# Kernel tuning notes

Hardware: AMD Instinct MI355X
Metric: run time of the kernel (lower is better)

Reference implementation:

```python
import jax, jax.numpy as jnp
import numpy as np

N, E, F = 50000, 400000, 32

_WN = ["w10","w11","w20","w21","w30","w31","w40","w41","wl01","wl02","wl1","wl2"]
_BN = ["b10","b11","b20","b21","b30","b31","b40","b41","bl01","bl02","bl1","bl2"]
_DIMS = [(4,F),(F,F),(2*F+F+4,F),(F,F),(6*F,F),(F,F),(6*F,F),(F,F),(F,F),(F,F),(F,4),(F,1)]


def _lin(key, fin, fout):
    kw, kb = jax.random.split(key)
    w = jax.random.normal(kw, (fin, fout), jnp.float32) / np.float32(np.sqrt(fin))
    b = jax.random.normal(kb, (fout,), jnp.float32) * 0.01
    return w, b


def setup_inputs() -> dict:
    key = jax.random.key(0)
    ks = jax.random.split(key, 5)
    inp = {}
    inp["x"] = jax.random.normal(ks[0], (N, 4), jnp.float32)
    inp["edge_index"] = jax.random.randint(ks[1], (2, E), 0, N, jnp.int32)
    inp["edge_attr"] = jax.random.normal(ks[2], (E, 4), jnp.float32)
    inp["beta"] = jax.random.normal(ks[3], (N, 3), jnp.float32)
    lkeys = jax.random.split(ks[4], len(_DIMS))
    for i, (fin, fout) in enumerate(_DIMS):
        w, b = _lin(lkeys[i], fin, fout)
        inp[_WN[i]] = w
        inp[_BN[i]] = b
    return inp


def reference(x, edge_index, edge_attr, beta,
              w10, b10, w11, b11, w20, b20, w21, b21,
              w30, b30, w31, b31, w40, b40, w41, b41,
              wl01, bl01, wl02, bl02, wl1, bl1, wl2, bl2):
    row, col = edge_index[0], edge_index[1]
    n = x.shape[0]

    def mlp2(m, w0, b0, w1, b1):
        return jax.nn.relu(m @ w0 + b0) @ w1 + b1

    def seg_mean(h):  # scatter-mean onto target nodes (row), dim_size=n
        s = jax.ops.segment_sum(h, row, num_segments=n)
        c = jax.ops.segment_sum(jnp.ones((h.shape[0], 1), h.dtype), row, num_segments=n)
        return s / jnp.maximum(c, 1.0)

    # conv1: x is zeros with dim 4 (<=5), so message = mlp0(edge_attr)
    e1 = mlp2(edge_attr, w10, b10, w11, b11)            # [E,32]
    x1 = jax.nn.relu(seg_mean(e1)); e1 = jax.nn.relu(e1)
    # conv2
    ea2 = jnp.concatenate([edge_attr, e1], axis=1)      # [E,36]
    e2 = mlp2(jnp.concatenate([x1[row], x1[col], ea2], axis=1), w20, b20, w21, b21)
    x2 = jax.nn.relu(seg_mean(e2)); e2 = jax.nn.relu(e2)
    # conv3
    x21 = jnp.concatenate([x2, x1], axis=1)             # [N,64]
    ea3 = jnp.concatenate([e2, e1], axis=1)             # [E,64]
    e3 = mlp2(jnp.concatenate([x21[row], x21[col], ea3], axis=1), w30, b30, w31, b31)
    x3 = jax.nn.relu(seg_mean(e3)); e3 = jax.nn.relu(e3)
    # conv4 (node aggregate x4 is never used downstream, so skipped)
    x32 = jnp.concatenate([x3, x2], axis=1)
    ea4 = jnp.concatenate([e3, e2], axis=1)
    e4 = jax.nn.relu(mlp2(jnp.concatenate([x32[row], x32[col], ea4], axis=1), w40, b40, w41, b41))
    # heads
    out01 = e4 @ wl01 + bl01
    out02 = e4 @ wl02 + bl02
    edge_x = out01 @ wl1 + bl1 + edge_attr
    edge_x = edge_x / jnp.maximum(jnp.linalg.norm(edge_x, axis=1, keepdims=True), 1e-12)
    probs = jax.nn.sigmoid(out02 @ wl2 + bl2)           # [E,1]
    return (probs, edge_x, beta)
```

## Files before the change

### kernel.cpp

```cpp
#include <hip/hip_runtime.h>
#include <hip/hip_bf16.h>

#define EE 400000
#define NN 50000
#define SCAN_NBLK ((NN + 1023) / 1024)
#define NTILES (EE / 16)
#define TPX (NTILES / 8)
#define NPTILES ((NN + 15) / 16)
#define INIT_NBLK ((NN + 255) / 256)

typedef float f32x4 __attribute__((ext_vector_type(4)));
typedef __bf16 bf16x8 __attribute__((ext_vector_type(8)));
typedef unsigned int u32;
typedef unsigned int u32x4 __attribute__((ext_vector_type(4)));

static __device__ __forceinline__ bf16x8 u4_as_bf8(u32x4 u) {
  return __builtin_bit_cast(bf16x8, u);
}
static __device__ __forceinline__ u32 relu_pk2(u32 d) {
  u32 m = (d & 0x80008000u) >> 15;
  m ^= 0x00010001u;
  return d & ((m << 16) - m);
}
static __device__ __forceinline__ u32 pk2bf(float a, float b) {
  union { __bf16 h[2]; u32 w; } t;
  t.h[0] = (__bf16)a; t.h[1] = (__bf16)b;
  return t.w;
}

__global__ void init_pack_kernel(const float* __restrict__ w10, const float* __restrict__ w11,
                                 const float* __restrict__ w20, const float* __restrict__ w21,
                                 const float* __restrict__ w30, const float* __restrict__ w31,
                                 const float* __restrict__ w40, const float* __restrict__ w41,
                                 const float* __restrict__ wl01, const float* __restrict__ wl1,
                                 const float* __restrict__ wl02, const float* __restrict__ wl2,
                                 const float* __restrict__ bl01, const float* __restrict__ bl02,
                                 const float* __restrict__ bl1, const float* __restrict__ bl2,
                                 __bf16* __restrict__ pk,
                                 int* __restrict__ count, float* __restrict__ headw) {
  const int t = threadIdx.x;
  if (blockIdx.x >= 43) {
    int i = (blockIdx.x - 43) * 256 + t;
    if (i < NN) count[i] = 0;
    if (blockIdx.x == 43) {
      if (t < 4) {
        float s = bl1[t];
        for (int j = 0; j < 32; ++j) s += bl01[j] * wl1[j * 4 + t];
        headw[160 + t] = s;
      } else if (t == 4) {
        float s = bl2[0];
        for (int j = 0; j < 32; ++j) s += bl02[j] * wl2[j];
        headw[164] = s;
      }
    }
    return;
  }
  const int f = blockIdx.x;
  int stage, lf;
  const float *W0, *W1;
  if (f < 4)       { stage = 1; lf = f;      W0 = w10; W1 = w11; }
  else if (f < 14) { stage = 2; lf = f - 4;  W0 = w20; W1 = w21; }
  else if (f < 28) { stage = 3; lf = f - 14; W0 = w30; W1 = w31; }
  else             { stage = 4; lf = f - 28; W0 = w40; W1 = w41; }
#pragma unroll
  for (int u = 0; u < 2; ++u) {
    int idx = t * 2 + u;
    int lane = idx >> 3, i = idx & 7;
    int l15 = lane & 15, g = lane >> 4;
    int k = 8 * g + i;
    float v = 0.f;
    if (stage == 1) {
      if (lf < 2)      v = (k < 4) ? W0[k * 32 + lf * 16 + l15] : 0.f;
      else             v = W1[k * 32 + (lf - 2) * 16 + l15];
    } else if (stage == 2) {
      if (lf < 4)      { int part = lf >> 1, nb = lf & 1; v = W0[(part * 32 + k) * 32 + nb * 16 + l15]; }
      else if (lf < 6) { int nb = lf - 4; v = (k < 4) ? W0[(64 + k) * 32 + nb * 16 + l15] : 0.f; }
      else if (lf < 8) { int nb = lf - 6; v = W0[(68 + k) * 32 + nb * 16 + l15]; }
      else             { int nb = lf - 8; v = W1[k * 32 + nb * 16 + l15]; }
    } else {
      if (lf < 8)       { int part = lf >> 2, kb = (lf >> 1) & 1, nb = lf & 1;
                          v = W0[(part * 64 + kb * 32 + k) * 32 + nb * 16 + l15]; }
      else if (lf < 12) { int eb = (lf - 8) >> 1, nb = lf & 1;
                          v = W0[(128 + eb * 32 + k) * 32 + nb * 16 + l15]; }
      else if (lf < 14) { int nb = lf - 12; v = W1[k * 32 + nb * 16 + l15]; }
      else {
        if (l15 < 4)      { float s = 0.f; for (int j = 0; j < 32; ++j) s += wl01[k * 32 + j] * wl1[j * 4 + l15]; v = s; }
        else if (l15 == 4){ float s = 0.f; for (int j = 0; j < 32; ++j) s += wl02[k * 32 + j] * wl2[j]; v = s; }
      }
    }
    pk[f * 512 + idx] = (__bf16)v;
  }
}

__global__ void hist_kernel(const int* __restrict__ rowi, int* __restrict__ count) {
  int e = blockIdx.x * blockDim.x + threadIdx.x;
  if (e < EE) atomicAdd(&count[rowi[e]], 1);
}

__global__ void scanA_kernel(const int* __restrict__ count, int* __restrict__ offs,
                             int* __restrict__ partial) {
  __shared__ int lds[1024];
  const int t = threadIdx.x;
  const int i = blockIdx.x * 1024 + t;
  int v = (i < NN) ? count[i] : 0;
  lds[t] = v;
  __syncthreads();
  for (int off = 1; off < 1024; off <<= 1) {
    int u = (t >= off) ? lds[t - off] : 0;
    __syncthreads();
    lds[t] += u;
    __syncthreads();
  }
  int incl = lds[t];
  if (i < NN) offs[i] = incl - v;
  if (t == 1023) partial[blockIdx.x] = incl;
}

__global__ void scanB_kernel(const int* __restrict__ partial, int* __restrict__ offs,
                             int* __restrict__ cursor) {
  __shared__ int sbase;
  const int t = threadIdx.x;
  const int b = blockIdx.x;
  if (t < 64) {
    int s = 0;
    for (int j = t; j < b; j += 64) s += partial[j];
#pragma unroll
    for (int o = 32; o > 0; o >>= 1) s += __shfl_down(s, o);
    if (t == 0) sbase = s;
  }
  __syncthreads();
  const int base = sbase;
  const int i = b * 1024 + t;
  if (i < NN) {
    int o = offs[i] + base;
    offs[i] = o;
    cursor[i] = o;
  }
  if (b == 0 && t == 0) offs[NN] = EE;
}

__global__ void scatter_kernel(const int* __restrict__ rowi, const int* __restrict__ coli,
                               const float* __restrict__ eattr, int* __restrict__ cursor,
                               uint4* __restrict__ record, int* __restrict__ inv) {
  int e = blockIdx.x * blockDim.x + threadIdx.x;
  if (e >= EE) return;
  int r = rowi[e];
  int p = atomicAdd(&cursor[r], 1);
  inv[e] = p;
  const float4 v = *(const float4*)(eattr + (size_t)e * 4);
  uint4 rec;
  rec.x = (u32)r;
  rec.y = (u32)coli[e];
  rec.z = pk2bf(v.x, v.y);
  rec.w = pk2bf(v.z, v.w);
  record[p] = rec;
}

__global__ void agg_kernel(const __bf16* __restrict__ esrc,
                           const int* __restrict__ offs,
                           __bf16* __restrict__ dst1, int s1, int o1,
                           __bf16* __restrict__ dst2, int s2, int o2) {
  int idx = blockIdx.x * blockDim.x + threadIdx.x;
  int n = idx >> 5;
  int j = idx & 31;
  if (n >= NN) return;
  int a = offs[n], b = offs[n + 1];
  float s = 0.f;
  for (int t = a; t < b; ++t)
    s += (float)esrc[(size_t)t * 32 + j];
  float mean = s / fmaxf((float)(b - a), 1.f);
  __bf16 x = (__bf16)fmaxf(mean, 0.f);
  dst1[(size_t)n * s1 + o1 + j] = x;
  if (dst2) dst2[(size_t)n * s2 + o2 + j] = x;
}

template <int NPK>
__launch_bounds__(256, 4)
__global__ void nodeproj_kernel(const __bf16* __restrict__ pk,
                                const __bf16* __restrict__ xcat, int xoff, int xstride,
                                __bf16* __restrict__ ur, __bf16* __restrict__ uc) {
  constexpr int NKB = NPK / 32;
  const int tid = threadIdx.x;
  const int lane = tid & 63;
  const int wid = tid >> 6;
  const int l15 = lane & 15;
  const int g = lane >> 4;

  bf16x8 Br[NKB][2], Bc[NKB][2];
#pragma unroll
  for (int kb = 0; kb < NKB; ++kb)
#pragma unroll
    for (int nb = 0; nb < 2; ++nb) {
      Br[kb][nb] = *(const bf16x8*)(pk + (size_t)((0 * NKB + kb) * 2 + nb) * 512 + lane * 8);
      Bc[kb][nb] = *(const bf16x8*)(pk + (size_t)((1 * NKB + kb) * 2 + nb) * 512 + lane * 8);
    }

  const int t = blockIdx.x * 4 + wid;
  if (t >= NPTILES) return;
  const int base = t * 16;
  const int n = base + l15;
  const int nc = (n < NN) ? n : (NN - 1);

  f32x4 r0 = {0,0,0,0}, r1 = {0,0,0,0}, c0 = {0,0,0,0}, c1 = {0,0,0,0};
#pragma unroll
  for (int kb = 0; kb < NKB; ++kb) {
    bf16x8 a = *(const bf16x8*)(xcat + (size_t)nc * xstride + xoff + kb * 32 + 8 * g);
    r0 = __builtin_amdgcn_mfma_f32_16x16x32_bf16(a, Br[kb][0], r0, 0, 0, 0);
    r1 = __builtin_amdgcn_mfma_f32_16x16x32_bf16(a, Br[kb][1], r1, 0, 0, 0);
    c0 = __builtin_amdgcn_mfma_f32_16x16x32_bf16(a, Bc[kb][0], c0, 0, 0, 0);
    c1 = __builtin_amdgcn_mfma_f32_16x16x32_bf16(a, Bc[kb][1], c1, 0, 0, 0);
  }
#pragma unroll
  for (int r = 0; r < 4; ++r) {
    int m = 4 * g + r;
    if (base + m < NN) {
      size_t row = (size_t)(base + m) * 32;
      ur[row + l15]      = (__bf16)r0[r];
      ur[row + 16 + l15] = (__bf16)r1[r];
      uc[row + l15]      = (__bf16)c0[r];
      uc[row + 16 + l15] = (__bf16)c1[r];
    }
  }
}

template <int STAGE>
__launch_bounds__(256, 5)
__global__ void conv_kernel(const __bf16* __restrict__ pk,
                            const float* __restrict__ B0, const float* __restrict__ B1v,
                            const uint4* __restrict__ record,
                            const __bf16* __restrict__ ur,
                            const __bf16* __restrict__ uc,
                            const __bf16* __restrict__ ein1,
                            const __bf16* __restrict__ ein2,
                            __bf16* __restrict__ d1,
                            const float* __restrict__ headw,
                            float* __restrict__ tmpP, float* __restrict__ tmpEX) {
  constexpr int NEB  = (STAGE == 1) ? 1 : 2;
  constexpr int FEB  = (STAGE == 1) ? 0 : (STAGE == 2) ? 4 : 8;
  constexpr int FW1  = (STAGE == 1) ? 2 : (STAGE == 2) ? 8 : 12;
  __shared__ __align__(16) float ldsH[4 * 16 * 36];

  const int tid = threadIdx.x;
  const int lane = tid & 63;
  const int wid = tid >> 6;
  const int l15 = lane & 15;
  const int g = lane >> 4;

  bf16x8 Bf[NEB][2];
#pragma unroll
  for (int eb = 0; eb < NEB; ++eb)
#pragma unroll
    for (int nb = 0; nb < 2; ++nb)
      Bf[eb][nb] = *(const bf16x8*)(pk + (size_t)(FEB + eb * 2 + nb) * 512 + lane * 8);
  bf16x8 B2f[2];
#pragma unroll
  for (int nb = 0; nb < 2; ++nb)
    B2f[nb] = *(const bf16x8*)(pk + (size_t)(FW1 + nb) * 512 + lane * 8);

  bf16x8 I0, I1;
#pragma unroll
  for (int i = 0; i < 8; ++i) {
    int k = 8 * g + i;
    I0[i] = (k == l15)      ? (__bf16)1.0f : (__bf16)0.0f;
    I1[i] = (k == 16 + l15) ? (__bf16)1.0f : (__bf16)0.0f;
  }

  const float b0j0 = B0[l15], b0j1 = B0[l15 + 16];
  const float b1j0 = B1v[l15], b1j1 = B1v[l15 + 16];

  bf16x8 Bh;
  float bexc = 0.f, bp = 0.f;
  if (STAGE == 4) {
    Bh = *(const bf16x8*)(pk + (size_t)14 * 512 + lane * 8);
    if (l15 < 4) bexc = headw[160 + l15];
    bp = headw[164];
  }

  float* hl = &ldsH[wid * 576];

  const int xcd = blockIdx.x & 7;
  const int wloc = (blockIdx.x >> 3) * 4 + wid;
  const int nwl = (gridDim.x >> 3) * 4;
  for (int t0 = wloc; t0 < TPX; t0 += nwl) {
    const int t = xcd * TPX + t0;
    const int base = t * 16;
    const int p = base + l15;

    const uint4 rec = record[p];

    bf16x8 urf, ucf;
    if (STAGE >= 2) {
      int rid = (int)rec.x, cid = (int)rec.y;
      urf = *(const bf16x8*)(ur + (size_t)rid * 32 + 8 * g);
      ucf = *(const bf16x8*)(uc + (size_t)cid * 32 + 8 * g);
    }

    bf16x8 ae;
    if (STAGE <= 2) {
      u32x4 u = {0, 0, 0, 0};
      if (g == 0) { u.x = rec.z; u.y = rec.w; }
      ae = u4_as_bf8(u);
    }

    f32x4 a0a = {0,0,0,0}, a0b = {0,0,0,0}, a1a = {0,0,0,0}, a1b = {0,0,0,0};
    if (STAGE >= 2) {
      a0a = __builtin_amdgcn_mfma_f32_16x16x32_bf16(urf, I0, a0a, 0, 0, 0);
      a1a = __builtin_amdgcn_mfma_f32_16x16x32_bf16(urf, I1, a1a, 0, 0, 0);
      a0a = __builtin_amdgcn_mfma_f32_16x16x32_bf16(ucf, I0, a0a, 0, 0, 0);
      a1a = __builtin_amdgcn_mfma_f32_16x16x32_bf16(ucf, I1, a1a, 0, 0, 0);
    }
#pragma unroll
    for (int eb = 0; eb < NEB; ++eb) {
      bf16x8 a;
      if (STAGE == 1) {
        a = ae;
      } else if (STAGE == 2) {
        if (eb == 0) a = ae;
        else {
          u32x4 u = *(const u32x4*)(ein1 + (size_t)p * 32 + 8 * g);
          u.x = relu_pk2(u.x); u.y = relu_pk2(u.y); u.z = relu_pk2(u.z); u.w = relu_pk2(u.w);
          a = u4_as_bf8(u);
        }
      } else {
        const __bf16* src = (eb == 0) ? ein1 : ein2;
        u32x4 u = *(const u32x4*)(src + (size_t)p * 32 + 8 * g);
        u.x = relu_pk2(u.x); u.y = relu_pk2(u.y); u.z = relu_pk2(u.z); u.w = relu_pk2(u.w);
        a = u4_as_bf8(u);
      }
      a0b = __builtin_amdgcn_mfma_f32_16x16x32_bf16(a, Bf[eb][0], a0b, 0, 0, 0);
      a1b = __builtin_amdgcn_mfma_f32_16x16x32_bf16(a, Bf[eb][1], a1b, 0, 0, 0);
    }
    f32x4 acc0 = a0a + a0b, acc1 = a1a + a1b;

#pragma unroll
    for (int r = 0; r < 4; ++r) {
      int m = 4 * g + r;
      hl[m * 36 + l15]      = fmaxf(acc0[r] + b0j0, 0.f);
      hl[m * 36 + l15 + 16] = fmaxf(acc1[r] + b0j1, 0.f);
    }
    f32x4 h0 = *(const f32x4*)&hl[l15 * 36 + 8 * g];
    f32x4 h1 = *(const f32x4*)&hl[l15 * 36 + 8 * g + 4];
    bf16x8 a2;
#pragma unroll
    for (int i = 0; i < 4; ++i) { a2[i] = (__bf16)h0[i]; a2[i + 4] = (__bf16)h1[i]; }
    f32x4 o0 = {0,0,0,0}, o1 = {0,0,0,0};
    o0 = __builtin_amdgcn_mfma_f32_16x16x32_bf16(a2, B2f[0], o0, 0, 0, 0);
    o1 = __builtin_amdgcn_mfma_f32_16x16x32_bf16(a2, B2f[1], o1, 0, 0, 0);

    if (STAGE <= 3) {
#pragma unroll
      for (int r = 0; r < 4; ++r) {
        int m = 4 * g + r;
        size_t eo = (size_t)(base + m) * 32;
        d1[eo + l15]      = (__bf16)(o0[r] + b1j0);
        d1[eo + l15 + 16] = (__bf16)(o1[r] + b1j1);
      }
    } else {
#pragma unroll
      for (int r = 0; r < 4; ++r) {
        int m = 4 * g + r;
        hl[m * 36 + l15]      = fmaxf(o0[r] + b1j0, 0.f);
        hl[m * 36 + l15 + 16] = fmaxf(o1[r] + b1j1, 0.f);
      }
      f32x4 q0 = *(const f32x4*)&hl[l15 * 36 + 8 * g];
      f32x4 q1 = *(const f32x4*)&hl[l15 * 36 + 8 * g + 4];
      bf16x8 a3;
#pragma unroll
      for (int i = 0; i < 4; ++i) { a3[i] = (__bf16)q0[i]; a3[i + 4] = (__bf16)q1[i]; }
      f32x4 ho = {0,0,0,0};
      ho = __builtin_amdgcn_mfma_f32_16x16x32_bf16(a3, Bh, ho, 0, 0, 0);
#pragma unroll
      for (int r = 0; r < 4; ++r) {
        int m = 4 * g + r;
        int po = base + m;
        float s = ho[r];
        u32 zz = __shfl(rec.z, m);
        u32 ww = __shfl(rec.w, m);
        float v = 0.f, sq = 0.f;
        if (l15 < 4) {
          u32 wzw = (l15 & 2) ? ww : zz;
          u32 bits = (l15 & 1) ? (wzw & 0xffff0000u) : (wzw << 16);
          v = s + bexc + __uint_as_float(bits);
          sq = v * v;
        }
        sq += __shfl_xor(sq, 1);
        sq += __shfl_xor(sq, 2);
        if (l15 < 4) tmpEX[(size_t)po * 4 + l15] = v * (1.f / fmaxf(sqrtf(sq), 1e-12f));
        if (l15 == 4) tmpP[po] = 1.f / (1.f + __expf(-(s + bp)));
      }
    }
  }
}

__global__ void unpermute_kernel(const int* __restrict__ inv,
                                 const float* __restrict__ tmpP,
                                 const float* __restrict__ tmpEX,
                                 const float* __restrict__ beta,
                                 float* __restrict__ outP, float* __restrict__ outEX,
                                 float* __restrict__ outB) {
  int e = blockIdx.x * blockDim.x + threadIdx.x;
  if (e >= EE) return;
  int p = inv[e];
  outP[e] = tmpP[p];
  float4 ex = *(const float4*)(tmpEX + (size_t)p * 4);
  *(float4*)(outEX + (size_t)e * 4) = ex;
  if (e < NN * 3) outB[e] = beta[e];
}

extern "C" void kernel_launch(void* const* d_in, const int* in_sizes, int n_in,
                              void* d_out, int out_size, void* d_ws, size_t ws_size,
                              hipStream_t stream) {
  const float* eattr = (const float*)d_in[2];
  const float* beta = (const float*)d_in[3];
  const float* w10 = (const float*)d_in[4];  const float* b10 = (const float*)d_in[5];
  const float* w11 = (const float*)d_in[6];  const float* b11 = (const float*)d_in[7];
  const float* w20 = (const float*)d_in[8];  const float* b20 = (const float*)d_in[9];
  const float* w21 = (const float*)d_in[10]; const float* b21 = (const float*)d_in[11];
  const float* w30 = (const float*)d_in[12]; const float* b30 = (const float*)d_in[13];
  const float* w31 = (const float*)d_in[14]; const float* b31 = (const float*)d_in[15];
  const float* w40 = (const float*)d_in[16]; const float* b40 = (const float*)d_in[17];
  const float* w41 = (const float*)d_in[18]; const float* b41 = (const float*)d_in[19];
  const float* wl01 = (const float*)d_in[20]; const float* bl01 = (const float*)d_in[21];
  const float* wl02 = (const float*)d_in[22]; const float* bl02 = (const float*)d_in[23];
  const float* wl1 = (const float*)d_in[24];  const float* bl1 = (const float*)d_in[25];
  const float* wl2 = (const float*)d_in[26];  const float* bl2 = (const float*)d_in[27];
  const int* rowi = (const int*)d_in[1];
  const int* coli = rowi + EE;

  char* w = (char*)d_ws;
  auto alloc = [&](size_t bytes) {
    char* p = w;
    w += (bytes + 255) & ~(size_t)255;
    return p;
  };
  __bf16* e1b = (__bf16*)alloc((size_t)EE * 32 * 2);
  __bf16* e2b = (__bf16*)alloc((size_t)EE * 32 * 2);
  __bf16* e3b = (__bf16*)alloc((size_t)EE * 32 * 2);
  __bf16* ur  = (__bf16*)alloc((size_t)NN * 32 * 2);
  __bf16* uc  = (__bf16*)alloc((size_t)NN * 32 * 2);
  __bf16* x21 = (__bf16*)alloc((size_t)NN * 64 * 2);
  __bf16* x32 = (__bf16*)alloc((size_t)NN * 64 * 2);
  int* count = (int*)alloc(NN * 4);
  int* offs = (int*)alloc((NN + 1) * 4);
  int* cursor = (int*)alloc(NN * 4);
  int* inv = (int*)alloc(EE * 4);
  uint4* record = (uint4*)alloc((size_t)EE * 16);
  float* tmpP = (float*)alloc((size_t)EE * 4);
  float* tmpEX = (float*)alloc((size_t)EE * 4 * 4);
  float* headw = (float*)alloc(256 * 4);
  int* partial = (int*)alloc(512 * 4);
  __bf16* packw = (__bf16*)alloc((size_t)43 * 512 * 2);

  float* outP = (float*)d_out;
  float* outEX = outP + EE;
  float* outB = outP + (size_t)5 * EE;

  __bf16* pk1 = packw;
  __bf16* pk2 = packw + 4 * 512;
  __bf16* pk3 = packw + 14 * 512;
  __bf16* pk4 = packw + 28 * 512;

  init_pack_kernel<<<43 + INIT_NBLK, 256, 0, stream>>>(
      w10, w11, w20, w21, w30, w31, w40, w41, wl01, wl1, wl02, wl2,
      bl01, bl02, bl1, bl2, packw, count, headw);
  hist_kernel<<<(EE + 255) / 256, 256, 0, stream>>>(rowi, count);
  scanA_kernel<<<SCAN_NBLK, 1024, 0, stream>>>(count, offs, partial);
  scanB_kernel<<<SCAN_NBLK, 1024, 0, stream>>>(partial, offs, cursor);
  scatter_kernel<<<(EE + 255) / 256, 256, 0, stream>>>(rowi, coli, eattr, cursor,
                                                       record, inv);

  conv_kernel<1><<<2048, 256, 0, stream>>>(pk1, b10, b11, record,
                                           (const __bf16*)nullptr, (const __bf16*)nullptr,
                                           (const __bf16*)nullptr, (const __bf16*)nullptr, e1b,
                                           (const float*)nullptr, (float*)nullptr, (float*)nullptr);
  agg_kernel<<<(NN * 32 + 255) / 256, 256, 0, stream>>>(e1b, offs, x21, 64, 32,
                                                        (__bf16*)nullptr, 0, 0);
  nodeproj_kernel<32><<<(NPTILES + 3) / 4, 256, 0, stream>>>(pk2, x21, 32, 64, ur, uc);
  conv_kernel<2><<<2048, 256, 0, stream>>>(pk2, b20, b21, record,
                                           ur, uc, e1b, (const __bf16*)nullptr, e2b,
                                           (const float*)nullptr, (float*)nullptr, (float*)nullptr);
  agg_kernel<<<(NN * 32 + 255) / 256, 256, 0, stream>>>(e2b, offs, x21, 64, 0, x32, 64, 32);
  nodeproj_kernel<64><<<(NPTILES + 3) / 4, 256, 0, stream>>>(pk3, x21, 0, 64, ur, uc);
  conv_kernel<3><<<2048, 256, 0, stream>>>(pk3, b30, b31, record,
                                           ur, uc, e2b, e1b, e3b,
                                           (const float*)nullptr, (float*)nullptr, (float*)nullptr);
  agg_kernel<<<(NN * 32 + 255) / 256, 256, 0, stream>>>(e3b, offs, x32, 64, 0,
                                                        (__bf16*)nullptr, 0, 0);
  nodeproj_kernel<64><<<(NPTILES + 3) / 4, 256, 0, stream>>>(pk4, x32, 0, 64, ur, uc);
  conv_kernel<4><<<2048, 256, 0, stream>>>(pk4, b40, b41, record,
                                           ur, uc, e3b, e2b, (__bf16*)nullptr,
                                           headw, tmpP, tmpEX);
  unpermute_kernel<<<(EE + 255) / 256, 256, 0, stream>>>(inv, tmpP, tmpEX, beta,
                                                         outP, outEX, outB);
}
```

Measured before the change: 200.6 us.

## Fuse segment-mean aggregation with node projection into one kernel

Merges the per-node scatter-mean aggregation and the MFMA node projection into a single aggproj kernel. Freshly aggregated features stay in shared memory as the first K-block, and the older features are read from separate per-layer buffers instead of concatenated 64-wide arrays. This removes three kernel launches and a global round trip of the aggregated features. In exchange, only two of the four waves do the projection, and the tail bounds checks are dropped because NN is divisible by 16.

```diff
diff --git a/kernel.cpp b/kernel.cpp
--- a/kernel.cpp
+++ b/kernel.cpp
@@ -6,7 +6,7 @@
 #define SCAN_NBLK ((NN + 1023) / 1024)
 #define NTILES (EE / 16)
 #define TPX (NTILES / 8)
-#define NPTILES ((NN + 15) / 16)
+#define NPTILES (NN / 16)
 #define INIT_NBLK ((NN + 255) / 256)
 
 typedef float f32x4 __attribute__((ext_vector_type(4)));
@@ -156,70 +156,63 @@
   record[p] = rec;
 }
 
-__global__ void agg_kernel(const __bf16* __restrict__ esrc,
-                           const int* __restrict__ offs,
-                           __bf16* __restrict__ dst1, int s1, int o1,
-                           __bf16* __restrict__ dst2, int s2, int o2) {
-  int idx = blockIdx.x * blockDim.x + threadIdx.x;
-  int n = idx >> 5;
-  int j = idx & 31;
-  if (n >= NN) return;
-  int a = offs[n], b = offs[n + 1];
-  float s = 0.f;
-  for (int t = a; t < b; ++t)
-    s += (float)esrc[(size_t)t * 32 + j];
-  float mean = s / fmaxf((float)(b - a), 1.f);
-  __bf16 x = (__bf16)fmaxf(mean, 0.f);
-  dst1[(size_t)n * s1 + o1 + j] = x;
-  if (dst2) dst2[(size_t)n * s2 + o2 + j] = x;
-}
-
-template <int NPK>
+template <int NKB>
 __launch_bounds__(256, 4)
-__global__ void nodeproj_kernel(const __bf16* __restrict__ pk,
-                                const __bf16* __restrict__ xcat, int xoff, int xstride,
-                                __bf16* __restrict__ ur, __bf16* __restrict__ uc) {
-  constexpr int NKB = NPK / 32;
-  const int tid = threadIdx.x;
-  const int lane = tid & 63;
-  const int wid = tid >> 6;
+__global__ void aggproj_kernel(const __bf16* __restrict__ esrc,
+                               const int* __restrict__ offs,
+                               const __bf16* __restrict__ pk,
+                               const __bf16* __restrict__ xold,
+                               __bf16* __restrict__ xfresh,
+                               __bf16* __restrict__ ur, __bf16* __restrict__ uc) {
+  __shared__ __align__(16) float hl[16 * 36];
+  const int t = threadIdx.x;
+  const int base = blockIdx.x * 16;
+
+#pragma unroll
+  for (int q = 0; q < 2; ++q) {
+    int idx = q * 256 + t;
+    int nl = idx >> 5, j = idx & 31;
+    int n = base + nl;
+    int a = offs[n], b = offs[n + 1];
+    float s = 0.f;
+    for (int e = a; e < b; ++e)
+      s += (float)esrc[(size_t)e * 32 + j];
+    float x = fmaxf(s / fmaxf((float)(b - a), 1.f), 0.f);
+    hl[nl * 36 + j] = x;
+    xfresh[(size_t)n * 32 + j] = (__bf16)x;
+  }
+  __syncthreads();
+
+  const int lane = t & 63;
+  const int wid = t >> 6;
+  if (wid >= 2) return;
   const int l15 = lane & 15;
   const int g = lane >> 4;
 
-  bf16x8 Br[NKB][2], Bc[NKB][2];
-#pragma unroll
-  for (int kb = 0; kb < NKB; ++kb)
-#pragma unroll
-    for (int nb = 0; nb < 2; ++nb) {
-      Br[kb][nb] = *(const bf16x8*)(pk + (size_t)((0 * NKB + kb) * 2 + nb) * 512 + lane * 8);
-      Bc[kb][nb] = *(const bf16x8*)(pk + (size_t)((1 * NKB + kb) * 2 + nb) * 512 + lane * 8);
-    }
-
-  const int t = blockIdx.x * 4 + wid;
-  if (t >= NPTILES) return;
-  const int base = t * 16;
-  const int n = base + l15;
-  const int nc = (n < NN) ? n : (NN - 1);
-
-  f32x4 r0 = {0,0,0,0}, r1 = {0,0,0,0}, c0 = {0,0,0,0}, c1 = {0,0,0,0};
+  f32x4 o0 = {0, 0, 0, 0}, o1 = {0, 0, 0, 0};
 #pragma unroll
   for (int kb = 0; kb < NKB; ++kb) {
-    bf16x8 a = *(const bf16x8*)(xcat + (size_t)nc * xstride + xoff + kb * 32 + 8 * g);
-    r0 = __builtin_amdgcn_mfma_f32_16x16x32_bf16(a, Br[kb][0], r0, 0, 0, 0);
-    r1 = __builtin_amdgcn_mfma_f32_16x16x32_bf16(a, Br[kb][1], r1, 0, 0, 0);
-    c0 = __builtin_amdgcn_mfma_f32_16x16x32_bf16(a, Bc[kb][0], c0, 0, 0, 0);
-    c1 = __builtin_amdgcn_mfma_f32_16x16x32_bf16(a, Bc[kb][1], c1, 0, 0, 0);
-  }
+    bf16x8 Bf0 = *(const bf16x8*)(pk + (size_t)((wid * NKB + kb) * 2 + 0) * 512 + lane * 8);
+    bf16x8 Bf1 = *(const bf16x8*)(pk + (size_t)((wid * NKB + kb) * 2 + 1) * 512 + lane * 8);
+    bf16x8 a;
+    if (kb == 0) {
+      f32x4 h0 = *(const f32x4*)&hl[l15 * 36 + 8 * g];
+      f32x4 h1 = *(const f32x4*)&hl[l15 * 36 + 8 * g + 4];
+#pragma unroll
+      for (int i = 0; i < 4; ++i) { a[i] = (__bf16)h0[i]; a[i + 4] = (__bf16)h1[i]; }
+    } else {
+      a = *(const bf16x8*)(xold + (size_t)(base + l15) * 32 + 8 * g);
+    }
+    o0 = __builtin_amdgcn_mfma_f32_16x16x32_bf16(a, Bf0, o0, 0, 0, 0);
+    o1 = __builtin_amdgcn_mfma_f32_16x16x32_bf16(a, Bf1, o1, 0, 0, 0);
+  }
+  __bf16* dst = (wid == 0) ? ur : uc;
 #pragma unroll
   for (int r = 0; r < 4; ++r) {
     int m = 4 * g + r;
-    if (base + m < NN) {
-      size_t row = (size_t)(base + m) * 32;
-      ur[row + l15]      = (__bf16)r0[r];
-      ur[row + 16 + l15] = (__bf16)r1[r];
-      uc[row + l15]      = (__bf16)c0[r];
-      uc[row + 16 + l15] = (__bf16)c1[r];
-    }
+    size_t row = (size_t)(base + m) * 32;
+    dst[row + l15]      = (__bf16)o0[r];
+    dst[row + 16 + l15] = (__bf16)o1[r];
   }
 }
 
@@ -438,8 +431,9 @@
   __bf16* e3b = (__bf16*)alloc((size_t)EE * 32 * 2);
   __bf16* ur  = (__bf16*)alloc((size_t)NN * 32 * 2);
   __bf16* uc  = (__bf16*)alloc((size_t)NN * 32 * 2);
-  __bf16* x21 = (__bf16*)alloc((size_t)NN * 64 * 2);
-  __bf16* x32 = (__bf16*)alloc((size_t)NN * 64 * 2);
+  __bf16* x1b = (__bf16*)alloc((size_t)NN * 32 * 2);
+  __bf16* x2b = (__bf16*)alloc((size_t)NN * 32 * 2);
+  __bf16* x3b = (__bf16*)alloc((size_t)NN * 32 * 2);
   int* count = (int*)alloc(NN * 4);
   int* offs = (int*)alloc((NN + 1) * 4);
   int* cursor = (int*)alloc(NN * 4);
@@ -473,20 +467,16 @@
                                            (const __bf16*)nullptr, (const __bf16*)nullptr,
                                            (const __bf16*)nullptr, (const __bf16*)nullptr, e1b,
                                            (const float*)nullptr, (float*)nullptr, (float*)nullptr);
-  agg_kernel<<<(NN * 32 + 255) / 256, 256, 0, stream>>>(e1b, offs, x21, 64, 32,
-                                                        (__bf16*)nullptr, 0, 0);
-  nodeproj_kernel<32><<<(NPTILES + 3) / 4, 256, 0, stream>>>(pk2, x21, 32, 64, ur, uc);
+  aggproj_kernel<1><<<NPTILES, 256, 0, stream>>>(e1b, offs, pk2,
+                                                 (const __bf16*)nullptr, x1b, ur, uc);
   conv_kernel<2><<<2048, 256, 0, stream>>>(pk2, b20, b21, record,
                                            ur, uc, e1b, (const __bf16*)nullptr, e2b,
                                            (const float*)nullptr, (float*)nullptr, (float*)nullptr);
-  agg_kernel<<<(NN * 32 + 255) / 256, 256, 0, stream>>>(e2b, offs, x21, 64, 0, x32, 64, 32);
-  nodeproj_kernel<64><<<(NPTILES + 3) / 4, 256, 0, stream>>>(pk3, x21, 0, 64, ur, uc);
+  aggproj_kernel<2><<<NPTILES, 256, 0, stream>>>(e2b, offs, pk3, x1b, x2b, ur, uc);
   conv_kernel<3><<<2048, 256, 0, stream>>>(pk3, b30, b31, record,
                                            ur, uc, e2b, e1b, e3b,
                                            (const float*)nullptr, (float*)nullptr, (float*)nullptr);
-  agg_kernel<<<(NN * 32 + 255) / 256, 256, 0, stream>>>(e3b, offs, x32, 64, 0,
-                                                        (__bf16*)nullptr, 0, 0);
-  nodeproj_kernel<64><<<(NPTILES + 3) / 4, 256, 0, stream>>>(pk4, x32, 0, 64, ur, uc);
+  aggproj_kernel<2><<<NPTILES, 256, 0, stream>>>(e3b, offs, pk4, x2b, x3b, ur, uc);
   conv_kernel<4><<<2048, 256, 0, stream>>>(pk4, b40, b41, record,
                                            ur, uc, e3b, e2b, (__bf16*)nullptr,
                                            headw, tmpP, tmpEX);
```

Result: faster. 193.4 us, median of 2 (-3.6%).
